# Kernel optimization log

Hardware: AMD Instinct MI355X
Metric: run time of the kernel (lower is better)

The kernel has to match this reference:

```python
import jax, jax.numpy as jnp
import numpy as np

N, D, H = 32768, 512, 8
HD = D // H  # head_dim = 64
LN_EPS = 1e-5


def setup_inputs() -> dict:
    key = jax.random.key(0)
    ks = jax.random.split(key, 5)
    s = 1.0 / np.sqrt(D)
    return {
        "h": jax.random.normal(ks[0], (N, D), dtype=jnp.float32),
        "Wq": jax.random.normal(ks[1], (D, D), dtype=jnp.float32) * s,
        "Wk": jax.random.normal(ks[2], (D, D), dtype=jnp.float32) * s,
        "Wv": jax.random.normal(ks[3], (D, D), dtype=jnp.float32) * s,
        "Wf": jax.random.normal(ks[4], (D, D), dtype=jnp.float32) * s,
        "ln_gamma": jnp.ones((D,), dtype=jnp.float32),
        "ln_beta": jnp.zeros((D,), dtype=jnp.float32),
    }


def _layernorm(x, g, b):
    mu = jnp.mean(x, axis=-1, keepdims=True)
    var = jnp.mean(jnp.square(x - mu), axis=-1, keepdims=True)
    return (x - mu) * jax.lax.rsqrt(var + LN_EPS) * g + b


def reference(h, Wq, Wk, Wv, Wf, ln_gamma, ln_beta):
    n = h.shape[0]
    # projections (torch Linear y = x @ W^T; weights here stored as [in,out])
    q = jax.nn.relu((h @ Wq).reshape(n, H, HD))
    k = jax.nn.relu((h @ Wk).reshape(n, H, HD))
    v = (h @ Wv).reshape(n, H, HD)
    # per-node outer-product accumulation over heads (n = head axis here)
    kv = jnp.einsum('bnd,bne->bde', k, v)          # [N, HD, HD]
    num = jnp.einsum('bnd,bde->bne', q, kv)        # [N, H, HD]
    denom = jnp.einsum('bnd,bd->bn', q, k.sum(axis=1))  # [N, H]
    attn = num / denom[..., None]                  # [N, H, HD]
    fh = attn.reshape(n, D) @ Wf                   # dropout = identity (eval)
    out = _layernorm(h + fh, ln_gamma, ln_beta)
    return (out, q, k, v)
```

## Files before the change

kernel.cpp:

```cpp
#include <hip/hip_runtime.h>
#include <hip/hip_bf16.h>

#define NROWS 32768
#define DIM   512
#define HEADS 8
#define LN_EPS 1e-5f

typedef __attribute__((ext_vector_type(8))) short short8;
typedef __attribute__((ext_vector_type(4))) float floatx4;

typedef __attribute__((address_space(3))) void lds_void;
typedef __attribute__((address_space(1))) void gbl_void;

__device__ __forceinline__ void async16(const void* g, void* l) {
    __builtin_amdgcn_global_load_lds(
        (gbl_void*)(unsigned long long)(uintptr_t)g,
        (lds_void*)(unsigned int)(uintptr_t)l,
        16, 0, 0);
}

__global__ __launch_bounds__(256) void hconv_kernel(
    const float* __restrict__ h, __hip_bfloat16* __restrict__ hb)
{
    const size_t i = ((size_t)blockIdx.x * 256 + threadIdx.x) * 4;
    const float4 f = *(const float4*)(h + i);
    union { ushort4 u; __hip_bfloat16 b[4]; } pk;
    pk.b[0] = __float2bfloat16(f.x);
    pk.b[1] = __float2bfloat16(f.y);
    pk.b[2] = __float2bfloat16(f.z);
    pk.b[3] = __float2bfloat16(f.w);
    *(ushort4*)(hb + i) = pk.u;
}

__global__ __launch_bounds__(256) void wtrans_kernel(
    const float* __restrict__ W, __hip_bfloat16* __restrict__ Wt)
{
    __shared__ float tile[32][33];
    const int bn = blockIdx.x * 32;
    const int bk = blockIdx.y * 32;
    const int tx = threadIdx.x & 31;
    const int ty = threadIdx.x >> 5;
    #pragma unroll
    for (int i = ty; i < 32; i += 8)
        tile[i][tx] = W[(size_t)(bk + i) * DIM + bn + tx];
    __syncthreads();
    #pragma unroll
    for (int i = ty; i < 32; i += 8)
        Wt[(size_t)(bn + i) * DIM + bk + tx] = __float2bfloat16(tile[tx][i]);
}

__global__ __launch_bounds__(256) void mfma_gemm_kernel(
    const __hip_bfloat16* __restrict__ A,
    const __hip_bfloat16* __restrict__ Bt,
    float* __restrict__ C, int relu)
{
    __shared__ __align__(16) char smem[16384];

    const int t    = threadIdx.x;
    const int lane = t & 63;
    const int w    = t >> 6;
    const int wm   = w >> 1, wn = w & 1;
    const int l16  = lane & 15, quad = lane >> 4;
    const int bm   = blockIdx.y * 128;
    const int bn   = blockIdx.x * 128;

    const int c0 = w * 128 + lane;
    const int c1 = c0 + 64;
    const int r0 = c0 >> 2, kq0 = (c0 & 3) ^ ((r0 >> 1) & 3);
    const int r1 = c1 >> 2, kq1 = (c1 & 3) ^ ((r1 >> 1) & 3);

    const __hip_bfloat16* gA0 = A  + (size_t)(bm + r0) * DIM + kq0 * 8;
    const __hip_bfloat16* gA1 = A  + (size_t)(bm + r1) * DIM + kq1 * 8;
    const __hip_bfloat16* gB0 = Bt + (size_t)(bn + r0) * DIM + kq0 * 8;
    const __hip_bfloat16* gB1 = Bt + (size_t)(bn + r1) * DIM + kq1 * 8;

    char* dA0 = smem + (w * 128 +  0) * 16;
    char* dA1 = smem + (w * 128 + 64) * 16;
    char* dB0 = smem + 8192 + (w * 128 +  0) * 16;
    char* dB1 = smem + 8192 + (w * 128 + 64) * 16;

    int aoff[4], boff[4];
    #pragma unroll
    for (int i = 0; i < 4; ++i) {
        const int ra = wm * 64 + i * 16 + l16;
        aoff[i] = (ra * 4 + (quad ^ ((ra >> 1) & 3))) * 16;
        const int rb = wn * 64 + i * 16 + l16;
        boff[i] = 8192 + (rb * 4 + (quad ^ ((rb >> 1) & 3))) * 16;
    }

    floatx4 acc[4][4];
    #pragma unroll
    for (int i = 0; i < 4; ++i)
        #pragma unroll
        for (int j = 0; j < 4; ++j)
            acc[i][j] = (floatx4){0.f, 0.f, 0.f, 0.f};

    for (int k0 = 0; k0 < DIM; k0 += 32) {
        async16(gA0 + k0, dA0);
        async16(gA1 + k0, dA1);
        async16(gB0 + k0, dB0);
        async16(gB1 + k0, dB1);
        __syncthreads();

        short8 af[4], bf[4];
        #pragma unroll
        for (int i = 0; i < 4; ++i) af[i] = *(const short8*)(smem + aoff[i]);
        #pragma unroll
        for (int j = 0; j < 4; ++j) bf[j] = *(const short8*)(smem + boff[j]);

        #pragma unroll
        for (int i = 0; i < 4; ++i)
            #pragma unroll
            for (int j = 0; j < 4; ++j)
                acc[i][j] = __builtin_amdgcn_mfma_f32_16x16x32_bf16(
                    af[i], bf[j], acc[i][j], 0, 0, 0);

        __syncthreads();
    }

    #pragma unroll
    for (int i = 0; i < 4; ++i) {
        const int gr = bm + wm * 64 + i * 16 + quad * 4;
        #pragma unroll
        for (int j = 0; j < 4; ++j) {
            const int gc = bn + wn * 64 + j * 16 + l16;
            #pragma unroll
            for (int rg = 0; rg < 4; ++rg) {
                float vv = acc[i][j][rg];
                if (relu) vv = fmaxf(vv, 0.f);
                C[(size_t)(gr + rg) * DIM + gc] = vv;
            }
        }
    }
}

__global__ __launch_bounds__(256) void attn_kernel(
    const float* __restrict__ q, const float* __restrict__ k,
    const float* __restrict__ v, __hip_bfloat16* __restrict__ attn)
{
    __shared__ float sq[2][DIM], sk[2][DIM], sv[2][DIM];
    __shared__ float skv[2][64][68];
    __shared__ float sksum[2][64];

    const int t = threadIdx.x;
    const int r = t >> 7;
    const int u = t & 127;
    const size_t base = ((size_t)blockIdx.x * 2 + r) * DIM;

    ((float4*)sq[r])[u] = ((const float4*)(q + base))[u];
    ((float4*)sk[r])[u] = ((const float4*)(k + base))[u];
    ((float4*)sv[r])[u] = ((const float4*)(v + base))[u];
    __syncthreads();

    const int e0 = (u & 15) * 4;
    const int d0 = (u >> 4) * 8;

    if (u < 64) {
        float s = 0.f;
        #pragma unroll
        for (int h = 0; h < HEADS; ++h) s += sk[r][h * 64 + u];
        sksum[r][u] = s;
    }

    float4 acc[8];
    #pragma unroll
    for (int i = 0; i < 8; ++i) acc[i] = make_float4(0.f, 0.f, 0.f, 0.f);
    #pragma unroll
    for (int h = 0; h < HEADS; ++h) {
        const float4 v4 = *(const float4*)&sv[r][h * 64 + e0];
        #pragma unroll
        for (int i = 0; i < 8; ++i) {
            const float kd = sk[r][h * 64 + d0 + i];
            acc[i].x += kd * v4.x; acc[i].y += kd * v4.y;
            acc[i].z += kd * v4.z; acc[i].w += kd * v4.w;
        }
    }
    #pragma unroll
    for (int i = 0; i < 8; ++i)
        *(float4*)&skv[r][d0 + i][e0] = acc[i];
    __syncthreads();

    const int n = u >> 4;
    float sx = 0.f, sy = 0.f, sz = 0.f, sw = 0.f, den = 0.f;
    #pragma unroll 8
    for (int d = 0; d < 64; ++d) {
        const float qd = sq[r][n * 64 + d];
        const float4 kv4 = *(const float4*)&skv[r][d][e0];
        sx += qd * kv4.x; sy += qd * kv4.y;
        sz += qd * kv4.z; sw += qd * kv4.w;
        den += qd * sksum[r][d];
    }
    union { ushort4 us; __hip_bfloat16 b[4]; } pk;
    pk.b[0] = __float2bfloat16(sx / den);
    pk.b[1] = __float2bfloat16(sy / den);
    pk.b[2] = __float2bfloat16(sz / den);
    pk.b[3] = __float2bfloat16(sw / den);
    *(ushort4*)(attn + base + n * 64 + e0) = pk.us;
}

__global__ __launch_bounds__(256) void ln_kernel(
    const float* __restrict__ h, const float* fh,
    const float* __restrict__ gamma, const float* __restrict__ beta,
    float* out)
{
    const int lane = threadIdx.x & 63;
    const int wave = threadIdx.x >> 6;
    const size_t base = ((size_t)blockIdx.x * 4 + wave) * DIM;

    float x[8];
    float s = 0.f;
    #pragma unroll
    for (int i = 0; i < 8; ++i) {
        const int j = lane + i * 64;
        x[i] = h[base + j] + fh[base + j];
        s += x[i];
    }
    #pragma unroll
    for (int off = 32; off > 0; off >>= 1) s += __shfl_down(s, off);
    const float mu = __shfl(s, 0) * (1.f / DIM);

    float vs = 0.f;
    #pragma unroll
    for (int i = 0; i < 8; ++i) { const float d = x[i] - mu; vs += d * d; }
    #pragma unroll
    for (int off = 32; off > 0; off >>= 1) vs += __shfl_down(vs, off);
    const float rstd = rsqrtf(__shfl(vs, 0) * (1.f / DIM) + LN_EPS);

    #pragma unroll
    for (int i = 0; i < 8; ++i) {
        const int j = lane + i * 64;
        out[base + j] = (x[i] - mu) * rstd * gamma[j] + beta[j];
    }
}

extern "C" void kernel_launch(void* const* d_in, const int* in_sizes, int n_in,
                              void* d_out, int out_size, void* d_ws, size_t ws_size,
                              hipStream_t stream)
{
    const float* h     = (const float*)d_in[0];
    const float* Wq    = (const float*)d_in[1];
    const float* Wk    = (const float*)d_in[2];
    const float* Wv    = (const float*)d_in[3];
    const float* Wf    = (const float*)d_in[4];
    const float* gamma = (const float*)d_in[5];
    const float* beta  = (const float*)d_in[6];

    const size_t ND = (size_t)NROWS * DIM;
    float* out = (float*)d_out;
    float* qo  = out + ND;
    float* ko  = out + 2 * ND;
    float* vo  = out + 3 * ND;
    float* fh  = out;

    __hip_bfloat16* hb  = (__hip_bfloat16*)d_ws;
    __hip_bfloat16* wtq = hb + ND;
    __hip_bfloat16* wtk = wtq + DIM * DIM;
    __hip_bfloat16* wtv = wtk + DIM * DIM;
    __hip_bfloat16* wtf = wtv + DIM * DIM;
    __hip_bfloat16* attnb = hb;

    const dim3 ggrid(DIM / 128, NROWS / 128);
    const dim3 wgrid(16, 16);

    hconv_kernel<<<NROWS * DIM / 1024, 256, 0, stream>>>(h, hb);
    wtrans_kernel<<<wgrid, 256, 0, stream>>>(Wq, wtq);
    wtrans_kernel<<<wgrid, 256, 0, stream>>>(Wk, wtk);
    wtrans_kernel<<<wgrid, 256, 0, stream>>>(Wv, wtv);
    wtrans_kernel<<<wgrid, 256, 0, stream>>>(Wf, wtf);

    mfma_gemm_kernel<<<ggrid, 256, 0, stream>>>(hb, wtq, qo, 1);
    mfma_gemm_kernel<<<ggrid, 256, 0, stream>>>(hb, wtk, ko, 1);
    mfma_gemm_kernel<<<ggrid, 256, 0, stream>>>(hb, wtv, vo, 0);

    attn_kernel<<<NROWS / 2, 256, 0, stream>>>(qo, ko, vo, attnb);

    mfma_gemm_kernel<<<ggrid, 256, 0, stream>>>(attnb, wtf, fh, 0);

    ln_kernel<<<NROWS / 4, 256, 0, stream>>>(h, fh, gamma, beta, out);
}
```

Measured before the change: 543.1 us.

## Fuse QKV projections into one launch with full-K LDS A-tile and direct B loads

Replaces the per-k-step double-sync GEMM with a kernel that loads a whole 64x512 A row-block into 64KB LDS once and streams B fragments straight from global memory. The Q, K and V projections run in a single launch, with the matrix chosen by blockIdx.x and ReLU applied per matrix through a bitmask. This removes the per-iteration barriers and two kernel launches. In exchange it uses heavy LDS (2 blocks/CU), reads B from global or L2 without LDS reuse, and relies on the weight matrices and outputs sitting contiguously in memory.

```diff
diff --git a/kernel.cpp b/kernel.cpp
--- a/kernel.cpp
+++ b/kernel.cpp
@@ -49,84 +49,79 @@
         Wt[(size_t)(bn + i) * DIM + bk + tx] = __float2bfloat16(tile[tx][i]);
 }
 
-__global__ __launch_bounds__(256) void mfma_gemm_kernel(
+__global__ __launch_bounds__(256, 2) void gemm_kernel(
     const __hip_bfloat16* __restrict__ A,
-    const __hip_bfloat16* __restrict__ Bt,
-    float* __restrict__ C, int relu)
-{
-    __shared__ __align__(16) char smem[16384];
+    const __hip_bfloat16* __restrict__ Bt_base,
+    float* __restrict__ C_base, int relu_mask)
+{
+    __shared__ __align__(16) char smem[65536];
 
     const int t    = threadIdx.x;
     const int lane = t & 63;
     const int w    = t >> 6;
-    const int wm   = w >> 1, wn = w & 1;
     const int l16  = lane & 15, quad = lane >> 4;
-    const int bm   = blockIdx.y * 128;
-    const int bn   = blockIdx.x * 128;
-
-    const int c0 = w * 128 + lane;
-    const int c1 = c0 + 64;
-    const int r0 = c0 >> 2, kq0 = (c0 & 3) ^ ((r0 >> 1) & 3);
-    const int r1 = c1 >> 2, kq1 = (c1 & 3) ^ ((r1 >> 1) & 3);
-
-    const __hip_bfloat16* gA0 = A  + (size_t)(bm + r0) * DIM + kq0 * 8;
-    const __hip_bfloat16* gA1 = A  + (size_t)(bm + r1) * DIM + kq1 * 8;
-    const __hip_bfloat16* gB0 = Bt + (size_t)(bn + r0) * DIM + kq0 * 8;
-    const __hip_bfloat16* gB1 = Bt + (size_t)(bn + r1) * DIM + kq1 * 8;
-
-    char* dA0 = smem + (w * 128 +  0) * 16;
-    char* dA1 = smem + (w * 128 + 64) * 16;
-    char* dB0 = smem + 8192 + (w * 128 +  0) * 16;
-    char* dB1 = smem + 8192 + (w * 128 + 64) * 16;
-
-    int aoff[4], boff[4];
+    const int mat  = blockIdx.x >> 1;
+    const int nb   = blockIdx.x & 1;
+    const int bm   = blockIdx.y * 64;
+    const int relu = (relu_mask >> mat) & 1;
+    const int nbase = nb * 256 + w * 64;
+
+    const __hip_bfloat16* Bt = Bt_base + (size_t)mat * DIM * DIM;
+    float* C = C_base + (size_t)mat * (size_t)NROWS * DIM;
+
+    #pragma unroll
+    for (int i = 0; i < 16; ++i) {
+        const int r = w * 16 + i;
+        async16(A + (size_t)(bm + r) * DIM + (lane ^ (r & 7)) * 8,
+                smem + r * 1024 + lane * 16);
+    }
+
+    const __hip_bfloat16* bptr[4];
+    #pragma unroll
+    for (int j = 0; j < 4; ++j)
+        bptr[j] = Bt + (size_t)(nbase + j * 16 + l16) * DIM + quad * 8;
+
+    int aoffE[4];
     #pragma unroll
     for (int i = 0; i < 4; ++i) {
-        const int ra = wm * 64 + i * 16 + l16;
-        aoff[i] = (ra * 4 + (quad ^ ((ra >> 1) & 3))) * 16;
-        const int rb = wn * 64 + i * 16 + l16;
-        boff[i] = 8192 + (rb * 4 + (quad ^ ((rb >> 1) & 3))) * 16;
-    }
-
-    floatx4 acc[4][4];
-    #pragma unroll
-    for (int i = 0; i < 4; ++i)
+        const int m = i * 16 + l16;
+        aoffE[i] = m * 1024 + ((quad ^ (m & 7)) & 7) * 16;
+    }
+
+    floatx4 acc[16];
+    #pragma unroll
+    for (int i = 0; i < 16; ++i) acc[i] = (floatx4){0.f, 0.f, 0.f, 0.f};
+
+    __syncthreads();
+
+    #pragma unroll 4
+    for (int kit = 0; kit < 16; ++kit) {
+        short8 bfv[4], af[4];
         #pragma unroll
         for (int j = 0; j < 4; ++j)
-            acc[i][j] = (floatx4){0.f, 0.f, 0.f, 0.f};
-
-    for (int k0 = 0; k0 < DIM; k0 += 32) {
-        async16(gA0 + k0, dA0);
-        async16(gA1 + k0, dA1);
-        async16(gB0 + k0, dB0);
-        async16(gB1 + k0, dB1);
-        __syncthreads();
-
-        short8 af[4], bf[4];
-        #pragma unroll
-        for (int i = 0; i < 4; ++i) af[i] = *(const short8*)(smem + aoff[i]);
-        #pragma unroll
-        for (int j = 0; j < 4; ++j) bf[j] = *(const short8*)(smem + boff[j]);
-
+            bfv[j] = *(const short8*)(bptr[j] + kit * 32);
+        #pragma unroll
+        for (int i = 0; i < 4; ++i)
+            af[i] = *(const short8*)(smem + ((aoffE[i] ^ ((kit & 1) << 6))
+                                             + (kit >> 1) * 128));
         #pragma unroll
         for (int i = 0; i < 4; ++i)
             #pragma unroll
             for (int j = 0; j < 4; ++j)
-                acc[i][j] = __builtin_amdgcn_mfma_f32_16x16x32_bf16(
-                    af[i], bf[j], acc[i][j], 0, 0, 0);
-
-        __syncthreads();
+                acc[i * 4 + j] = __builtin_amdgcn_mfma_f32_16x16x32_bf16(
+                    af[i], bfv[j], acc[i * 4 + j], 0, 0, 0);
     }
 
     #pragma unroll
     for (int i = 0; i < 4; ++i) {
-        const int gr = bm + wm * 64 + i * 16 + quad * 4;
+        const int gr = bm + i * 16 + quad * 4;
         #pragma unroll
         for (int j = 0; j < 4; ++j) {
-            const int gc = bn + wn * 64 + j * 16 + l16;
+            const int gc = nbase + j * 16 + l16;
+            floatx4 v = acc[i * 4 + j];
             #pragma unroll
             for (int rg = 0; rg < 4; ++rg) {
-                float vv = acc[i][j][rg];
+                float vv = v[rg];
                 if (relu) vv = fmaxf(vv, 0.f);
                 C[(size_t)(gr + rg) * DIM + gc] = vv;
             }
@@ -248,8 +243,6 @@
     const size_t ND = (size_t)NROWS * DIM;
     float* out = (float*)d_out;
     float* qo  = out + ND;
-    float* ko  = out + 2 * ND;
-    float* vo  = out + 3 * ND;
     float* fh  = out;
 
     __hip_bfloat16* hb  = (__hip_bfloat16*)d_ws;
@@ -259,7 +252,6 @@
     __hip_bfloat16* wtf = wtv + DIM * DIM;
     __hip_bfloat16* attnb = hb;
 
-    const dim3 ggrid(DIM / 128, NROWS / 128);
     const dim3 wgrid(16, 16);
 
     hconv_kernel<<<NROWS * DIM / 1024, 256, 0, stream>>>(h, hb);
@@ -268,13 +260,11 @@
     wtrans_kernel<<<wgrid, 256, 0, stream>>>(Wv, wtv);
     wtrans_kernel<<<wgrid, 256, 0, stream>>>(Wf, wtf);
 
-    mfma_gemm_kernel<<<ggrid, 256, 0, stream>>>(hb, wtq, qo, 1);
-    mfma_gemm_kernel<<<ggrid, 256, 0, stream>>>(hb, wtk, ko, 1);
-    mfma_gemm_kernel<<<ggrid, 256, 0, stream>>>(hb, wtv, vo, 0);
-
-    attn_kernel<<<NROWS / 2, 256, 0, stream>>>(qo, ko, vo, attnb);
-
-    mfma_gemm_kernel<<<ggrid, 256, 0, stream>>>(attnb, wtf, fh, 0);
+    gemm_kernel<<<dim3(6, NROWS / 64), 256, 0, stream>>>(hb, wtq, qo, 0x3);
+
+    attn_kernel<<<NROWS / 2, 256, 0, stream>>>(qo, qo + ND, qo + 2 * ND, attnb);
+
+    gemm_kernel<<<dim3(2, NROWS / 64), 256, 0, stream>>>(attnb, wtf, fh, 0x0);
 
     ln_kernel<<<NROWS / 4, 256, 0, stream>>>(h, fh, gamma, beta, out);
 }
```

After: 585.6 us. +7.8%, slower.
